# Performance work log

Measured on AMD Instinct MI355X. Metric: run time of the kernel, lower is better.

## Reference

```python
import jax, jax.numpy as jnp
import numpy as np

# static config (matches init_kwargs)
E = 1280          # n_embed
L = 4             # n_layer
NH = 16           # n_heads
D = E // NH       # head_dim = 80
M = 5120          # n_mlp
O = 2048          # n_output_embed
MS = 2            # spatial_merge_size
NGPS = 48         # sqrt(num_position_embeddings)
GRID_T, GRID_H, GRID_W = 1, 32, 32
N_IMG = 2
SPP = GRID_T * GRID_H * GRID_W   # 1024 tokens per image
S = N_IMG * SPP                  # 2048 total tokens
H4 = E * MS * MS                 # merger hidden = 5120
IN_PATCH = 3 * 2 * 16 * 16       # 1536
DS_IDX = [1, 2]


def _ln(x, w, b, eps=1e-6):
    m = x.mean(-1, keepdims=True)
    v = ((x - m) ** 2).mean(-1, keepdims=True)
    return (x - m) / jnp.sqrt(v + eps) * w + b


def _pos_embed_interp(pos_emb):
    # bilinear interpolation of the 48x48 learned grid to GRID_HxGRID_W, per image
    hi = jnp.linspace(0.0, NGPS - 1.0, GRID_H)
    wi = jnp.linspace(0.0, NGPS - 1.0, GRID_W)
    hf = hi.astype(jnp.int32); wf = wi.astype(jnp.int32)
    hc = jnp.minimum(hf + 1, NGPS - 1); wc = jnp.minimum(wf + 1, NGPS - 1)
    dh = hi - hf; dw = wi - wf
    idx = [(hf[:, None] * NGPS + wf[None]).ravel(), (hf[:, None] * NGPS + wc[None]).ravel(),
           (hc[:, None] * NGPS + wf[None]).ravel(), (hc[:, None] * NGPS + wc[None]).ravel()]
    wts = [((1 - dh)[:, None] * (1 - dw)[None]).ravel(), ((1 - dh)[:, None] * dw[None]).ravel(),
           (dh[:, None] * (1 - dw)[None]).ravel(), (dh[:, None] * dw[None]).ravel()]
    pe = sum(pos_emb[i] * w[:, None] for i, w in zip(idx, wts))  # [h*w, E]
    pe = jnp.tile(pe, (GRID_T, 1))
    # spatial-merge permutation: (t, h/m, m, w/m, m) -> (t, h/m, w/m, m, m)
    pe = pe.reshape(GRID_T, GRID_H // MS, MS, GRID_W // MS, MS, E).transpose(0, 1, 3, 2, 4, 5).reshape(-1, E)
    return jnp.tile(pe, (N_IMG, 1))  # [S, E]


def _rotary_freqs():
    dim = D // 2  # VisionRotaryEmbedding dim = 40
    inv = 1.0 / (10000.0 ** (jnp.arange(0, dim, 2, dtype=jnp.float32) / dim))  # [D//4]
    hp = jnp.broadcast_to(jnp.arange(GRID_H)[:, None], (GRID_H, GRID_W))
    hp = hp.reshape(GRID_H // MS, MS, GRID_W // MS, MS).transpose(0, 2, 1, 3).ravel()
    wp = jnp.broadcast_to(jnp.arange(GRID_W)[None, :], (GRID_H, GRID_W))
    wp = wp.reshape(GRID_H // MS, MS, GRID_W // MS, MS).transpose(0, 2, 1, 3).ravel()
    pos = jnp.stack([hp, wp], -1)            # [h*w, 2]
    pos = jnp.tile(pos, (GRID_T, 1))
    pos = jnp.tile(pos, (N_IMG, 1))          # [S, 2]
    table = jnp.arange(max(GRID_H, GRID_W), dtype=jnp.float32)[:, None] * inv[None]  # [G, D//4]
    return table[pos].reshape(S, -1)         # [S, D//2] (h-freqs || w-freqs)


def _rope(t, cos, sin):
    # t: [S, NH, D]; cos/sin: [S, 1, D]; applied in float32 as in the source
    t1, t2 = jnp.split(t, 2, axis=-1)
    rot = jnp.concatenate([-t2, t1], -1)
    return (t.astype(jnp.float32) * cos + rot.astype(jnp.float32) * sin).astype(t.dtype)


def _attn(x, qkv_w, qkv_b, pw, pb, cos, sin, mask):
    qkv = (x @ qkv_w.T + qkv_b).reshape(S, 3, NH, D)
    q, k, v = qkv[:, 0], qkv[:, 1], qkv[:, 2]
    q = _rope(q, cos, sin)
    k = _rope(k, cos, sin)
    scores = jnp.einsum('shd,thd->hst', q, k) / np.sqrt(D).astype(np.float32) + mask
    p = jax.nn.softmax(scores.astype(jnp.float32), axis=-1).astype(q.dtype)
    o = jnp.einsum('hst,thd->shd', p, v).reshape(S, E)
    return o @ pw.T + pb


def _merger(x, ln_w, ln_b, f1w, f1b, f2w, f2b, post):
    if post:
        x = _ln(x.reshape(-1, H4), ln_w, ln_b)
    else:
        x = _ln(x, ln_w, ln_b).reshape(-1, H4)
    h = jax.nn.gelu(x @ f1w.T + f1b, approximate=False)  # nn.GELU() exact
    return h @ f2w.T + f2b


def setup_inputs() -> dict:
    key = jax.random.key(0)
    ks = iter(jax.random.split(key, 24))
    n = lambda s: jax.random.normal(next(ks), s, dtype=jnp.float32) * 0.02
    return {
        'x': jax.random.normal(next(ks), (S, IN_PATCH), dtype=jnp.float32),
        'patch_w': n((E, IN_PATCH)), 'patch_b': jnp.zeros((E,), jnp.float32),
        'pos_emb': n((NGPS * NGPS, E)),
        'ln1_w': jnp.ones((L, E), jnp.float32), 'ln1_b': jnp.zeros((L, E), jnp.float32),
        'ln2_w': jnp.ones((L, E), jnp.float32), 'ln2_b': jnp.zeros((L, E), jnp.float32),
        'qkv_w': n((L, 3 * E, E)), 'qkv_b': jnp.zeros((L, 3 * E), jnp.float32),
        'attn_proj_w': n((L, E, E)), 'attn_proj_b': jnp.zeros((L, E), jnp.float32),
        'fc1_w': n((L, M, E)), 'fc1_b': jnp.zeros((L, M), jnp.float32),
        'fc2_w': n((L, E, M)), 'fc2_b': jnp.zeros((L, E), jnp.float32),
        'm_ln_w': jnp.ones((E,), jnp.float32), 'm_ln_b': jnp.zeros((E,), jnp.float32),
        'm_fc1_w': n((H4, H4)), 'm_fc1_b': jnp.zeros((H4,), jnp.float32),
        'm_fc2_w': n((O, H4)), 'm_fc2_b': jnp.zeros((O,), jnp.float32),
        'ds_ln_w': jnp.ones((2, H4), jnp.float32), 'ds_ln_b': jnp.zeros((2, H4), jnp.float32),
        'ds_fc1_w': n((2, H4, H4)), 'ds_fc1_b': jnp.zeros((2, H4), jnp.float32),
        'ds_fc2_w': n((2, O, H4)), 'ds_fc2_b': jnp.zeros((2, O), jnp.float32),
    }


def reference(x, patch_w, patch_b, pos_emb, ln1_w, ln1_b, ln2_w, ln2_b,
              qkv_w, qkv_b, attn_proj_w, attn_proj_b, fc1_w, fc1_b, fc2_w, fc2_b,
              m_ln_w, m_ln_b, m_fc1_w, m_fc1_b, m_fc2_w, m_fc2_b,
              ds_ln_w, ds_ln_b, ds_fc1_w, ds_fc1_b, ds_fc2_w, ds_fc2_b):
    # patch embed (Conv3d with kernel==stride == per-patch linear)
    h = x @ patch_w.T + patch_b                      # [S, E]
    h = h + _pos_embed_interp(pos_emb)
    freqs = _rotary_freqs()                          # [S, D//2]
    cos = jnp.concatenate([jnp.cos(freqs)] * 2, -1)[:, None, :]  # [S,1,D]
    sin = jnp.concatenate([jnp.sin(freqs)] * 2, -1)[:, None, :]
    img = jnp.arange(S) // SPP                       # cu_seqlens block-diagonal mask
    mask = jnp.where(img[:, None] == img[None, :], 0.0, jnp.finfo(jnp.float32).min)
    ds_feats = []
    for l in range(L):
        h = h + _attn(_ln(h, ln1_w[l], ln1_b[l]), qkv_w[l], qkv_b[l],
                      attn_proj_w[l], attn_proj_b[l], cos, sin, mask)
        hn = _ln(h, ln2_w[l], ln2_b[l])
        h = h + (jax.nn.gelu(hn @ fc1_w[l].T + fc1_b[l], approximate=True) @ fc2_w[l].T + fc2_b[l])
        if l in DS_IDX:
            j = DS_IDX.index(l)
            ds_feats.append(_merger(h, ds_ln_w[j], ds_ln_b[j], ds_fc1_w[j], ds_fc1_b[j],
                                    ds_fc2_w[j], ds_fc2_b[j], post=True))
    main = _merger(h, m_ln_w, m_ln_b, m_fc1_w, m_fc1_b, m_fc2_w, m_fc2_b, post=False)
    return jnp.stack([main] + ds_feats, 0)           # [3, S//4, O]
```

## Files before the change

### kernel.cpp

```cpp
#include <hip/hip_runtime.h>
#include <hip/hip_bf16.h>
#include <cstdio>
#include <cstdint>

#define E_    1280
#define L_    4
#define NH_   16
#define D_    80
#define DP_   96
#define MLP_  5120
#define O_    2048
#define S_    2048
#define H4_   5120
#define INP_  1536

typedef __attribute__((ext_vector_type(4))) float f32x4;
typedef __attribute__((ext_vector_type(8))) short short8v;
typedef __attribute__((ext_vector_type(4))) short short4v;

__device__ __forceinline__ short f2bf(float f){
  uint32_t u = __float_as_uint(f);
  uint32_t r = (u + 0x7FFFu + ((u >> 16) & 1u)) >> 16;
  return (short)r;
}
__device__ __forceinline__ float bf2f(short s){
  return __uint_as_float(((uint32_t)(uint16_t)s) << 16);
}
__device__ __forceinline__ float gelu_tanh(float x){
  return 0.5f*x*(1.f + tanhf(0.7978845608028654f*(x + 0.044715f*x*x*x)));
}
__device__ __forceinline__ float gelu_erf(float x){
  return 0.5f*x*(1.f + erff(x*0.7071067811865476f));
}
__device__ __forceinline__ void token_hw(int t, int& hc, int& wc){
  hc = ((t>>1)&1) + ((t>>6)<<1);
  wc = (t&1)      + (((t>>2)&15)<<1);
}

__device__ __forceinline__ void gload16(const short* g, short* l){
  __builtin_amdgcn_global_load_lds((const __attribute__((address_space(1))) void*)g,
                                   (__attribute__((address_space(3))) void*)l, 16, 0, 0);
}

struct CvtSeg { const float* src; short* dst; long long n; };
struct CvtP { CvtSeg s[10]; long long tot; };

__global__ __launch_bounds__(256)
void cvtall_k(CvtP p)
{
  const long long stride = (long long)gridDim.x*256*8;
  for (long long i = ((long long)blockIdx.x*256 + threadIdx.x)*8; i < p.tot; i += stride){
    long long off = i; int si = 0;
    #pragma unroll
    for (int k=0;k<9;k++){ if (off >= p.s[si].n){ off -= p.s[si].n; si++; } }
    const float* src = p.s[si].src + off;
    short* dst = p.s[si].dst + off;
    float4 v0 = *(const float4*)(src);
    float4 v1 = *(const float4*)(src+4);
    short8v w;
    w[0]=f2bf(v0.x); w[1]=f2bf(v0.y); w[2]=f2bf(v0.z); w[3]=f2bf(v0.w);
    w[4]=f2bf(v1.x); w[5]=f2bf(v1.y); w[6]=f2bf(v1.z); w[7]=f2bf(v1.w);
    *(short8v*)dst = w;
  }
}

struct Gemm2P {
  const short* A; const short* B; void* C;
  const float* bias;
  short* part;
  int lda, ldb, ldc, M, N, K;
  float scale;
  long long aOffH, aOffI, bOffH, bOffI, cOffH, cOffI;
  int nImg, kSplit;
};

template<int EPI, bool RES, bool CF32, bool SPLIT>
__global__ __launch_bounds__(256)
void gemm2_k(Gemm2P p)
{
  __shared__ short As[3][4096];
  __shared__ short Bs[3][4096];

  int z = blockIdx.z, ks = 0;
  if constexpr (SPLIT){ ks = z % p.kSplit; z /= p.kSplit; }
  const int hI = z / p.nImg, iI = z % p.nImg;
  const long long aB = (long long)hI*p.aOffH + (long long)iI*p.aOffI;
  const long long bB = (long long)hI*p.bOffH + (long long)iI*p.bOffI;
  const long long cB = (long long)hI*p.cOffH + (long long)iI*p.cOffI;

  const int nwg = gridDim.x*gridDim.y;
  const int orig = blockIdx.y*gridDim.x + blockIdx.x;
  const int q8 = nwg >> 3, r8 = nwg & 7;
  const int xcd = orig & 7, oidx = orig >> 3;
  const int wg = (xcd < r8 ? xcd*(q8+1) : r8*(q8+1) + (xcd-r8)*q8) + oidx;
  const int nt = wg % gridDim.x, mt = wg / gridDim.x;

  const int tid = threadIdx.x, lane = tid & 63, wv = tid >> 6;

  const int sr = lane >> 2;
  const int sc = (lane & 3) * 8;
  const int Kp  = SPLIT ? p.K / p.kSplit : p.K;
  const int kBeg = SPLIT ? ks * Kp : 0;
  int ra0 = mt*128 + (wv*2+0)*16 + sr; if (ra0 >= p.M) ra0 = p.M-1;
  int ra1 = mt*128 + (wv*2+1)*16 + sr; if (ra1 >= p.M) ra1 = p.M-1;
  int rb0 = nt*128 + (wv*2+0)*16 + sr; if (rb0 >= p.N) rb0 = p.N-1;
  int rb1 = nt*128 + (wv*2+1)*16 + sr; if (rb1 >= p.N) rb1 = p.N-1;
  const short* pa0 = p.A + aB + (long long)ra0*p.lda + sc + kBeg;
  const short* pa1 = p.A + aB + (long long)ra1*p.lda + sc + kBeg;
  const short* pb0 = p.B + bB + (long long)rb0*p.ldb + sc + kBeg;
  const short* pb1 = p.B + bB + (long long)rb1*p.ldb + sc + kBeg;
  const int so0 = (wv*2+0)*512;
  const int so1 = (wv*2+1)*512;

  const int fr = lane & 15, fo = (lane >> 4) * 8;
  const int wr = (wv >> 1) * 64, wc = (wv & 1) * 64;

  f32x4 acc[4][4] = {};

  auto stage = [&](int buf, int t){
    const int k0 = t << 5;
    gload16(pa0 + k0, &As[buf][so0]);
    gload16(pa1 + k0, &As[buf][so1]);
    gload16(pb0 + k0, &Bs[buf][so0]);
    gload16(pb1 + k0, &Bs[buf][so1]);
  };

  const int ntile = Kp >> 5;
  stage(0, 0);
  if (ntile > 1) stage(1, 1);
  for (int t = 0; t < ntile; t++){
    const int cur = t % 3;
    if (t + 1 < ntile) { asm volatile("s_waitcnt vmcnt(4)" ::: "memory"); }
    else               { asm volatile("s_waitcnt vmcnt(0)" ::: "memory"); }
    __builtin_amdgcn_s_barrier();
    asm volatile("" ::: "memory");
    short8v a[4], b[4];
    #pragma unroll
    for (int i=0;i<4;i++){
      a[i] = *(const short8v*)&As[cur][(wr + i*16 + fr)*32 + fo];
      b[i] = *(const short8v*)&Bs[cur][(wc + i*16 + fr)*32 + fo];
    }
    if (t + 2 < ntile) stage((t+2)%3, t+2);
    #pragma unroll
    for (int i=0;i<4;i++)
      #pragma unroll
      for (int j=0;j<4;j++)
        acc[i][j] = __builtin_amdgcn_mfma_f32_16x16x32_bf16(a[i], b[j], acc[i][j], 0, 0, 0);
  }

  #pragma unroll
  for (int i=0;i<4;i++){
    #pragma unroll
    for (int j=0;j<4;j++){
      #pragma unroll
      for (int r=0;r<4;r++){
        const int row = mt*128 + wr + i*16 + (lane>>4)*4 + r;
        const int col = nt*128 + wc + j*16 + fr;
        if (row < p.M && col < p.N){
          float v = acc[i][j][r];
          if constexpr (SPLIT){
            p.part[((long long)ks*p.M + row)*p.N + col] = f2bf(v);
          } else {
            if (p.bias) v += p.bias[col];
            if constexpr (EPI==1) v = gelu_tanh(v);
            if constexpr (EPI==2) v = gelu_erf(v);
            if constexpr (EPI==3) v *= p.scale;
            const long long off = cB + (long long)row*p.ldc + col;
            if constexpr (RES)  v += ((const float*)p.C)[off];
            if constexpr (CF32) ((float*)p.C)[off] = v;
            else                ((short*)p.C)[off] = f2bf(v);
          }
        }
      }
    }
  }
}

template<int EPI, bool RES, bool CF32>
__global__ __launch_bounds__(256)
void reduce_k(const short* __restrict__ part, int kSplit, long long MN, int N,
              const float* __restrict__ bias, void* __restrict__ C)
{
  const long long i = ((long long)blockIdx.x*256 + threadIdx.x)*8;
  if (i >= MN) return;
  float v[8];
  { short8v pv = *(const short8v*)(part + i);
    #pragma unroll
    for (int e=0;e<8;e++) v[e] = bf2f(pv[e]); }
  for (int ks = 1; ks < kSplit; ks++){
    short8v pv = *(const short8v*)(part + (long long)ks*MN + i);
    #pragma unroll
    for (int e=0;e<8;e++) v[e] += bf2f(pv[e]);
  }
  if (bias){
    const int col = (int)(i % N);
    #pragma unroll
    for (int e=0;e<8;e++) v[e] += bias[col+e];
  }
  #pragma unroll
  for (int e=0;e<8;e++){
    if constexpr (EPI==1) v[e] = gelu_tanh(v[e]);
    if constexpr (EPI==2) v[e] = gelu_erf(v[e]);
  }
  if constexpr (RES){
    const float* cp = (const float*)C + i;
    #pragma unroll
    for (int e=0;e<8;e++) v[e] += cp[e];
  }
  if constexpr (CF32){
    float4 o0 = {v[0],v[1],v[2],v[3]}, o1 = {v[4],v[5],v[6],v[7]};
    *(float4*)((float*)C + i) = o0;
    *(float4*)((float*)C + i + 4) = o1;
  } else {
    short8v o;
    #pragma unroll
    for (int e=0;e<8;e++) o[e] = f2bf(v[e]);
    *(short8v*)((short*)C + i) = o;
  }
}

__global__ __launch_bounds__(256)
void redln_k(const short* __restrict__ part, long long MN, const float* __restrict__ bias,
             float* __restrict__ h, const float* __restrict__ lnw, const float* __restrict__ lnb,
             short* __restrict__ aln)
{
  __shared__ float red[8];
  const int row = blockIdx.x, tid = threadIdx.x;
  float4 vals[2];
  float s = 0.f, sq = 0.f;
  #pragma unroll
  for (int it=0; it<2; it++){
    const int c = tid*4 + it*1024;
    if (c < E_){
      float4 v = *(const float4*)(h + (long long)row*E_ + c);
      const float4 b = *(const float4*)(bias + c);
      v.x += b.x; v.y += b.y; v.z += b.z; v.w += b.w;
      #pragma unroll
      for (int ks=0; ks<4; ks++){
        short4v pv = *(const short4v*)(part + (long long)ks*MN + (long long)row*E_ + c);
        v.x += bf2f(pv[0]); v.y += bf2f(pv[1]); v.z += bf2f(pv[2]); v.w += bf2f(pv[3]);
      }
      *(float4*)(h + (long long)row*E_ + c) = v;
      vals[it] = v;
      s  += v.x+v.y+v.z+v.w;
      sq += v.x*v.x+v.y*v.y+v.z*v.z+v.w*v.w;
    }
  }
  #pragma unroll
  for (int m=32;m;m>>=1){ s += __shfl_xor(s,m,64); sq += __shfl_xor(sq,m,64); }
  const int wv = tid>>6, lane = tid&63;
  if (lane==0){ red[wv]=s; red[4+wv]=sq; }
  __syncthreads();
  s  = red[0]+red[1]+red[2]+red[3];
  sq = red[4]+red[5]+red[6]+red[7];
  const float mean = s / (float)E_;
  const float var  = sq / (float)E_ - mean*mean;
  const float rs   = rsqrtf(var + 1e-6f);
  #pragma unroll
  for (int it=0; it<2; it++){
    const int c = tid*4 + it*1024;
    if (c < E_){
      const float4 v = vals[it];
      const float4 gw = *(const float4*)(lnw + c);
      const float4 bw = *(const float4*)(lnb + c);
      short4v o;
      o[0] = f2bf((v.x-mean)*rs*gw.x + bw.x);
      o[1] = f2bf((v.y-mean)*rs*gw.y + bw.y);
      o[2] = f2bf((v.z-mean)*rs*gw.z + bw.z);
      o[3] = f2bf((v.w-mean)*rs*gw.w + bw.w);
      *(short4v*)(aln + (long long)row*E_ + c) = o;
    }
  }
}

__global__ __launch_bounds__(256)
void fattn_k(const short* __restrict__ qh, const short* __restrict__ kh,
             const short* __restrict__ vt, short* __restrict__ o2)
{
  __shared__ short Ps[4][16*136];

  const int qt = blockIdx.x, h = blockIdx.y, img = blockIdx.z;
  const int tid = threadIdx.x, lane = tid & 63, wv = tid >> 6;
  const int fr = lane & 15, fo = (lane >> 4) * 8, g = lane >> 4;

  const short* qp = qh + ((long long)h*S_ + img*1024 + qt*64 + wv*16)*DP_;
  const short* kp = kh + ((long long)h*S_ + img*1024)*DP_;
  const short* vp = vt + ((long long)(h*2 + img))*80*1024;
  short* Pw = &Ps[wv][0];

  short8v q[3];
  #pragma unroll
  for (int t3=0;t3<3;t3++)
    q[t3] = *(const short8v*)(qp + (long long)fr*DP_ + t3*32 + fo);

  float m_[4], l_[4];
  f32x4 ao[5] = {};
  #pragma unroll
  for (int r=0;r<4;r++){ m_[r] = -3.0e38f; l_[r] = 0.f; }

  for (int t = 0; t < 8; t++){
    f32x4 sc[8] = {};
    #pragma unroll
    for (int j=0;j<8;j++){
      #pragma unroll
      for (int t3=0;t3<3;t3++){
        const short8v kb = *(const short8v*)(kp + (long long)(t*128 + j*16 + fr)*DP_ + t3*32 + fo);
        sc[j] = __builtin_amdgcn_mfma_f32_16x16x32_bf16(q[t3], kb, sc[j], 0,0,0);
      }
    }
    #pragma unroll
    for (int j=0;j<8;j++) sc[j] *= 0.11180339887498949f;

    #pragma unroll
    for (int r=0;r<4;r++){
      float mx = sc[0][r];
      #pragma unroll
      for (int j=1;j<8;j++) mx = fmaxf(mx, sc[j][r]);
      mx = fmaxf(mx, __shfl_xor(mx, 1, 64));
      mx = fmaxf(mx, __shfl_xor(mx, 2, 64));
      mx = fmaxf(mx, __shfl_xor(mx, 4, 64));
      mx = fmaxf(mx, __shfl_xor(mx, 8, 64));
      const float mn = fmaxf(m_[r], mx);
      const float al = __expf(m_[r] - mn);
      float ts = 0.f;
      #pragma unroll
      for (int j=0;j<8;j++){
        const float pv = __expf(sc[j][r] - mn);
        sc[j][r] = pv;
        ts += pv;
      }
      ts += __shfl_xor(ts, 1, 64);
      ts += __shfl_xor(ts, 2, 64);
      ts += __shfl_xor(ts, 4, 64);
      ts += __shfl_xor(ts, 8, 64);
      l_[r] = l_[r]*al + ts;
      m_[r] = mn;
      #pragma unroll
      for (int n=0;n<5;n++) ao[n][r] *= al;
      const int prow = g*4 + r;
      #pragma unroll
      for (int j=0;j<8;j++) Pw[prow*136 + j*16 + fr] = f2bf(sc[j][r]);
    }
    asm volatile("s_waitcnt lgkmcnt(0)" ::: "memory");
    __builtin_amdgcn_sched_barrier(0);

    #pragma unroll
    for (int t4=0;t4<4;t4++){
      const short8v pa = *(const short8v*)&Pw[fr*136 + t4*32 + fo];
      #pragma unroll
      for (int n=0;n<5;n++){
        const short8v vb = *(const short8v*)(vp + (long long)(n*16 + fr)*1024 + t*128 + t4*32 + fo);
        ao[n] = __builtin_amdgcn_mfma_f32_16x16x32_bf16(pa, vb, ao[n], 0,0,0);
      }
    }
  }

  short* op = o2 + ((long long)(img*1024 + qt*64 + wv*16))*E_ + h*80;
  #pragma unroll
  for (int r=0;r<4;r++){
    const float inv = 1.f / l_[r];
    const int row = g*4 + r;
    #pragma unroll
    for (int n=0;n<5;n++)
      op[(long long)row*E_ + n*16 + fr] = f2bf(ao[n][r] * inv);
  }
}

__global__ __launch_bounds__(256)
void ln_k(const float* __restrict__ X, const float* __restrict__ g, const float* __restrict__ bta,
          short* __restrict__ Y, int Cn)
{
  __shared__ float red[8];
  const int row = blockIdx.x;
  const float* x = X + (long long)row*Cn;
  short* y = Y + (long long)row*Cn;
  float s = 0.f, sq = 0.f;
  for (int c = threadIdx.x*4; c < Cn; c += 1024){
    float4 v = *(const float4*)(x + c);
    s  += v.x+v.y+v.z+v.w;
    sq += v.x*v.x+v.y*v.y+v.z*v.z+v.w*v.w;
  }
  #pragma unroll
  for (int m=32;m;m>>=1){ s += __shfl_xor(s,m,64); sq += __shfl_xor(sq,m,64); }
  const int wv = threadIdx.x>>6, lane = threadIdx.x&63;
  if (lane==0){ red[wv]=s; red[4+wv]=sq; }
  __syncthreads();
  s  = red[0]+red[1]+red[2]+red[3];
  sq = red[4]+red[5]+red[6]+red[7];
  const float mean = s / (float)Cn;
  const float var  = sq / (float)Cn - mean*mean;
  const float rs   = rsqrtf(var + 1e-6f);
  for (int c = threadIdx.x*4; c < Cn; c += 1024){
    float4 v  = *(const float4*)(x + c);
    float4 gw = *(const float4*)(g + c);
    float4 bw = *(const float4*)(bta + c);
    short4v o;
    o[0] = f2bf((v.x-mean)*rs*gw.x + bw.x);
    o[1] = f2bf((v.y-mean)*rs*gw.y + bw.y);
    o[2] = f2bf((v.z-mean)*rs*gw.z + bw.z);
    o[3] = f2bf((v.w-mean)*rs*gw.w + bw.w);
    *(short4v*)(y + c) = o;
  }
}

__global__ __launch_bounds__(256)
void rope_k(const short* __restrict__ qkv, short* __restrict__ qh,
            short* __restrict__ kh, short* __restrict__ vt)
{
  const int idx = blockIdx.x*256 + threadIdx.x;
  if (idx >= S_*NH_*40) return;
  const int d0 = idx % 40;
  const int h  = (idx / 40) % NH_;
  const int s  = idx / (40*NH_);
  const int t  = s & 1023, img = s >> 10;
  int hc, wc; token_hw(t, hc, wc);
  const int j  = d0 % 20;
  const float invf = exp2f(-0.66438561897747f * (float)j);
  const float pos  = (float)((d0 < 20) ? hc : wc);
  float sn, cs; sincosf(pos * invf, &sn, &cs);
  const short* base = qkv + (long long)s*3840 + h*80;
  const float q1 = bf2f(base[d0]),      q2 = bf2f(base[d0+40]);
  const float k1 = bf2f(base[1280+d0]), k2 = bf2f(base[1280+d0+40]);
  const long long qo = ((long long)h*S_ + s)*DP_;
  qh[qo + d0]    = f2bf(q1*cs - q2*sn);
  qh[qo + d0+40] = f2bf(q2*cs + q1*sn);
  kh[qo + d0]    = f2bf(k1*cs - k2*sn);
  kh[qo + d0+40] = f2bf(k2*cs + k1*sn);
  if (d0 < 16){ qh[qo + 80 + d0] = 0; kh[qo + 80 + d0] = 0; }
  const long long vo = (((long long)h*2 + img)*80)*1024 + t;
  vt[vo + (long long)d0*1024]      = base[2560+d0];
  vt[vo + (long long)(d0+40)*1024] = base[2560+d0+40];
}

__global__ __launch_bounds__(256)
void posadd_k(float* __restrict__ h, const float* __restrict__ pe)
{
  const int idx = blockIdx.x*256 + threadIdx.x;
  if (idx >= S_*(E_/4)) return;
  const int c4 = idx % (E_/4), s = idx / (E_/4);
  const int e = c4*4;
  const int t = s & 1023;
  int hc, wc; token_hw(t, hc, wc);
  const float hi = (float)hc * (47.f/31.f);
  const float wi = (float)wc * (47.f/31.f);
  int hf = (int)hi; float dh = hi - (float)hf; int h2 = min(hf+1, 47);
  int wf = (int)wi; float dw = wi - (float)wf; int w2 = min(wf+1, 47);
  const float w00=(1.f-dh)*(1.f-dw), w01=(1.f-dh)*dw, w10=dh*(1.f-dw), w11=dh*dw;
  const float4 a = *(const float4*)(pe + ((long long)(hf*48+wf))*E_ + e);
  const float4 b = *(const float4*)(pe + ((long long)(hf*48+w2))*E_ + e);
  const float4 c = *(const float4*)(pe + ((long long)(h2*48+wf))*E_ + e);
  const float4 d = *(const float4*)(pe + ((long long)(h2*48+w2))*E_ + e);
  float* out = h + (long long)s*E_ + e;
  float4 o = *(float4*)out;
  o.x += w00*a.x + w01*b.x + w10*c.x + w11*d.x;
  o.y += w00*a.y + w01*b.y + w10*c.y + w11*d.y;
  o.z += w00*a.z + w01*b.z + w10*c.z + w11*d.z;
  o.w += w00*a.w + w01*b.w + w10*c.w + w11*d.w;
  *(float4*)out = o;
}

static Gemm2P mk(const short* A, const short* B, void* C, const float* bias,
                 int lda, int ldb, int ldc, int M, int N, int K, float scale = 1.f)
{
  Gemm2P p{}; p.A=A; p.B=B; p.C=C; p.bias=bias; p.part=nullptr;
  p.lda=lda; p.ldb=ldb; p.ldc=ldc; p.M=M; p.N=N; p.K=K; p.scale=scale;
  p.aOffH=p.aOffI=p.bOffH=p.bOffI=p.cOffH=p.cOffI=0; p.nImg=1; p.kSplit=1;
  return p;
}

extern "C" void kernel_launch(void* const* d_in, const int* in_sizes, int n_in,
                              void* d_out, int out_size, void* d_ws, size_t ws_size,
                              hipStream_t stream)
{
  const float* x           = (const float*)d_in[0];
  const float* patch_w     = (const float*)d_in[1];
  const float* patch_b     = (const float*)d_in[2];
  const float* pos_emb     = (const float*)d_in[3];
  const float* ln1_w       = (const float*)d_in[4];
  const float* ln1_b       = (const float*)d_in[5];
  const float* ln2_w       = (const float*)d_in[6];
  const float* ln2_b       = (const float*)d_in[7];
  const float* qkv_w       = (const float*)d_in[8];
  const float* qkv_b       = (const float*)d_in[9];
  const float* attn_proj_w = (const float*)d_in[10];
  const float* attn_proj_b = (const float*)d_in[11];
  const float* fc1_w       = (const float*)d_in[12];
  const float* fc1_b       = (const float*)d_in[13];
  const float* fc2_w       = (const float*)d_in[14];
  const float* fc2_b       = (const float*)d_in[15];
  const float* m_ln_w      = (const float*)d_in[16];
  const float* m_ln_b      = (const float*)d_in[17];
  const float* m_fc1_w     = (const float*)d_in[18];
  const float* m_fc1_b     = (const float*)d_in[19];
  const float* m_fc2_w     = (const float*)d_in[20];
  const float* m_fc2_b     = (const float*)d_in[21];
  const float* ds_ln_w     = (const float*)d_in[22];
  const float* ds_ln_b     = (const float*)d_in[23];
  const float* ds_fc1_w    = (const float*)d_in[24];
  const float* ds_fc1_b    = (const float*)d_in[25];
  const float* ds_fc2_w    = (const float*)d_in[26];
  const float* ds_fc2_b    = (const float*)d_in[27];
  float* out = (float*)d_out;

  char* wsp = (char*)d_ws;
  auto alloc = [&](size_t bytes)->char*{
    char* p = wsp; wsp += (bytes + 255) & ~(size_t)255; return p;
  };
  float* h    = (float*)alloc((size_t)S_*E_*4);
  short* qkvb = (short*)alloc((size_t)S_*3840*2);
  short* aln  = (short*)alloc((size_t)S_*E_*2);
  short* qh   = (short*)alloc((size_t)NH_*S_*DP_*2);
  short* kh   = (short*)alloc((size_t)NH_*S_*DP_*2 + 4096);
  short* vt   = (short*)alloc((size_t)NH_*2*D_*1024*2 + 4096);
  short* part = (short*)alloc((size_t)24*1024*1024);
  short* o2   = (short*)alloc((size_t)S_*E_*2);
  short* ffn  = (short*)alloc((size_t)S_*MLP_*2);
  short* xb    = (short*)alloc((size_t)S_*INP_*2);
  short* pwB   = (short*)alloc((size_t)E_*INP_*2);
  short* qkvwB = (short*)alloc((size_t)L_*3840*E_*2);
  short* prwB  = (short*)alloc((size_t)L_*E_*E_*2);
  short* f1wB  = (short*)alloc((size_t)L_*MLP_*E_*2);
  short* f2wB  = (short*)alloc((size_t)L_*E_*MLP_*2);
  short* mf1B  = (short*)alloc((size_t)H4_*H4_*2);
  short* mf2B  = (short*)alloc((size_t)O_*H4_*2);
  short* df1B  = (short*)alloc((size_t)2*H4_*H4_*2);
  short* df2B  = (short*)alloc((size_t)2*O_*H4_*2);
  size_t need = (size_t)(wsp - (char*)d_ws);
  if (need > ws_size){
    fprintf(stderr, "kernel_launch: ws too small: need %zu have %zu\n", need, ws_size);
    return;
  }
  short* dsln = qkvb;

  const dim3 B256(256);

  { CvtP cp{};
    cp.s[0] = { x,         xb,    (long long)S_*INP_ };
    cp.s[1] = { patch_w,   pwB,   (long long)E_*INP_ };
    cp.s[2] = { qkv_w,     qkvwB, (long long)L_*3840*E_ };
    cp.s[3] = { attn_proj_w, prwB, (long long)L_*E_*E_ };
    cp.s[4] = { fc1_w,     f1wB,  (long long)L_*MLP_*E_ };
    cp.s[5] = { fc2_w,     f2wB,  (long long)L_*E_*MLP_ };
    cp.s[6] = { m_fc1_w,   mf1B,  (long long)H4_*H4_ };
    cp.s[7] = { m_fc2_w,   mf2B,  (long long)O_*H4_ };
    cp.s[8] = { ds_fc1_w,  df1B,  (long long)2*H4_*H4_ };
    cp.s[9] = { ds_fc2_w,  df2B,  (long long)2*O_*H4_ };
    cp.tot = 0;
    for (int i=0;i<10;i++) cp.tot += cp.s[i].n;
    cvtall_k<<<2048, B256, 0, stream>>>(cp); }

  auto G = [](int M, int N, int ks = 1){
    return dim3((unsigned)((N+127)/128), (unsigned)((M+127)/128), (unsigned)ks);
  };
  auto RG = [](long long MN){ return dim3((unsigned)((MN/8 + 255)/256)); };

  { Gemm2P pp = mk(xb, pwB, h, nullptr, INP_, INP_, E_, S_, E_, INP_);
    pp.part = part; pp.kSplit = 4;
    gemm2_k<0,false,true,true><<<G(S_,E_,4),B256,0,stream>>>(pp);
    reduce_k<0,false,true><<<RG((long long)S_*E_),B256,0,stream>>>(part, 4, (long long)S_*E_, E_, patch_b, h); }
  posadd_k<<<(S_*(E_/4)+255)/256, B256, 0, stream>>>(h, pos_emb);
  ln_k<<<S_, B256, 0, stream>>>(h, ln1_w, ln1_b, aln, E_);

  for (int l = 0; l < L_; l++){
    { Gemm2P pp = mk(aln, qkvwB + (size_t)l*3840*E_, qkvb, qkv_b + l*3840, E_, E_, 3840, S_, 3840, E_);
      gemm2_k<0,false,false,false><<<G(S_,3840),B256,0,stream>>>(pp); }
    rope_k<<<(S_*NH_*40+255)/256, B256, 0, stream>>>(qkvb, qh, kh, vt);
    fattn_k<<<dim3(16,16,2), B256, 0, stream>>>(qh, kh, vt, o2);
    { Gemm2P pp = mk(o2, prwB + (size_t)l*E_*E_, nullptr, nullptr, E_, E_, E_, S_, E_, E_);
      pp.part = part; pp.kSplit = 4;
      gemm2_k<0,false,true,true><<<G(S_,E_,4),B256,0,stream>>>(pp);
      redln_k<<<S_, B256, 0, stream>>>(part, (long long)S_*E_, attn_proj_b + l*E_,
                                       h, ln2_w + l*E_, ln2_b + l*E_, aln); }

    { Gemm2P pp = mk(aln, f1wB + (size_t)l*MLP_*E_, ffn, fc1_b + l*MLP_, E_, E_, MLP_, S_, MLP_, E_);
      gemm2_k<1,false,false,false><<<G(S_,MLP_),B256,0,stream>>>(pp); }
    { Gemm2P pp = mk(ffn, f2wB + (size_t)l*E_*MLP_, nullptr, nullptr, MLP_, MLP_, E_, S_, E_, MLP_);
      pp.part = part; pp.kSplit = 4;
      gemm2_k<0,false,true,true><<<G(S_,E_,4),B256,0,stream>>>(pp);
      const float* nw = (l < 3) ? (ln1_w + (l+1)*E_) : m_ln_w;
      const float* nb = (l < 3) ? (ln1_b + (l+1)*E_) : m_ln_b;
      redln_k<<<S_, B256, 0, stream>>>(part, (long long)S_*E_, fc2_b + l*E_, h, nw, nb, aln); }

    if (l == 1 || l == 2){
      const int j = l - 1;
      ln_k<<<512, B256, 0, stream>>>(h, ds_ln_w + (size_t)j*H4_, ds_ln_b + (size_t)j*H4_, dsln, H4_);
      { Gemm2P pp = mk(dsln, df1B + (size_t)j*H4_*H4_, ffn, nullptr, H4_, H4_, H4_, 512, H4_, H4_);
        pp.part = part; pp.kSplit = 4;
        gemm2_k<0,false,false,true><<<G(512,H4_,4),B256,0,stream>>>(pp);
        reduce_k<2,false,false><<<RG((long long)512*H4_),B256,0,stream>>>(part, 4, (long long)512*H4_, H4_, ds_fc1_b + (size_t)j*H4_, ffn); }
      { Gemm2P pp = mk(ffn, df2B + (size_t)j*O_*H4_, out + (size_t)(1+j)*512*O_, nullptr, H4_, H4_, O_, 512, O_, H4_);
        pp.part = part; pp.kSplit = 8;
        gemm2_k<0,false,true,true><<<G(512,O_,8),B256,0,stream>>>(pp);
        reduce_k<0,false,true><<<RG((long long)512*O_),B256,0,stream>>>(part, 8, (long long)512*O_, O_, ds_fc2_b + (size_t)j*O_, out + (size_t)(1+j)*512*O_); }
    }
  }

  { Gemm2P pp = mk(aln, mf1B, ffn, nullptr, H4_, H4_, H4_, 512, H4_, H4_);
    pp.part = part; pp.kSplit = 4;
    gemm2_k<0,false,false,true><<<G(512,H4_,4),B256,0,stream>>>(pp);
    reduce_k<2,false,false><<<RG((long long)512*H4_),B256,0,stream>>>(part, 4, (long long)512*H4_, H4_, m_fc1_b, ffn); }
  { Gemm2P pp = mk(ffn, mf2B, out, nullptr, H4_, H4_, O_, 512, O_, H4_);
    pp.part = part; pp.kSplit = 8;
    gemm2_k<0,false,true,true><<<G(512,O_,8),B256,0,stream>>>(pp);
    reduce_k<0,false,true><<<RG((long long)512*O_),B256,0,stream>>>(part, 8, (long long)512*O_, O_, m_fc2_b, out); }
}
```

Baseline: 1.779 ms.

## Split-K the QKV and FC1 GEMMs and split weight conversion per tensor

QKV and FC1 projections now run as 2-way split-K GEMMs writing bf16 partials, followed by a reduce kernel that applies bias (and GELU for FC1). The partial buffer is doubled to hold them. The single fused fp32->bf16 conversion kernel is replaced by one launch per tensor, and RoPE uses the fast __sincosf intrinsic. The aim is more parallelism and simpler conversion indexing, at the cost of extra partial-sum memory traffic, extra launches, and reduced sincos accuracy.

```diff
diff --git a/kernel.cpp b/kernel.cpp
--- a/kernel.cpp
+++ b/kernel.cpp
@@ -42,25 +42,17 @@
                                    (__attribute__((address_space(3))) void*)l, 16, 0, 0);
 }
 
-struct CvtSeg { const float* src; short* dst; long long n; };
-struct CvtP { CvtSeg s[10]; long long tot; };
-
-__global__ __launch_bounds__(256)
-void cvtall_k(CvtP p)
+__global__ __launch_bounds__(256)
+void cvt_k(const float* __restrict__ src, short* __restrict__ dst, long long n)
 {
   const long long stride = (long long)gridDim.x*256*8;
-  for (long long i = ((long long)blockIdx.x*256 + threadIdx.x)*8; i < p.tot; i += stride){
-    long long off = i; int si = 0;
-    #pragma unroll
-    for (int k=0;k<9;k++){ if (off >= p.s[si].n){ off -= p.s[si].n; si++; } }
-    const float* src = p.s[si].src + off;
-    short* dst = p.s[si].dst + off;
-    float4 v0 = *(const float4*)(src);
-    float4 v1 = *(const float4*)(src+4);
+  for (long long i = ((long long)blockIdx.x*256 + threadIdx.x)*8; i < n; i += stride){
+    float4 v0 = *(const float4*)(src+i);
+    float4 v1 = *(const float4*)(src+i+4);
     short8v w;
     w[0]=f2bf(v0.x); w[1]=f2bf(v0.y); w[2]=f2bf(v0.z); w[3]=f2bf(v0.w);
     w[4]=f2bf(v1.x); w[5]=f2bf(v1.y); w[6]=f2bf(v1.z); w[7]=f2bf(v1.w);
-    *(short8v*)dst = w;
+    *(short8v*)(dst+i) = w;
   }
 }
 
@@ -417,7 +409,8 @@
   const int j  = d0 % 20;
   const float invf = exp2f(-0.66438561897747f * (float)j);
   const float pos  = (float)((d0 < 20) ? hc : wc);
-  float sn, cs; sincosf(pos * invf, &sn, &cs);
+  float sn, cs;
+  __sincosf(pos * invf, &sn, &cs);
   const short* base = qkv + (long long)s*3840 + h*80;
   const float q1 = bf2f(base[d0]),      q2 = bf2f(base[d0+40]);
   const float k1 = bf2f(base[1280+d0]), k2 = bf2f(base[1280+d0+40]);
@@ -512,7 +505,7 @@
   short* qh   = (short*)alloc((size_t)NH_*S_*DP_*2);
   short* kh   = (short*)alloc((size_t)NH_*S_*DP_*2 + 4096);
   short* vt   = (short*)alloc((size_t)NH_*2*D_*1024*2 + 4096);
-  short* part = (short*)alloc((size_t)24*1024*1024);
+  short* part = (short*)alloc((size_t)48*1024*1024);
   short* o2   = (short*)alloc((size_t)S_*E_*2);
   short* ffn  = (short*)alloc((size_t)S_*MLP_*2);
   short* xb    = (short*)alloc((size_t)S_*INP_*2);
@@ -533,21 +526,20 @@
   short* dsln = qkvb;
 
   const dim3 B256(256);
-
-  { CvtP cp{};
-    cp.s[0] = { x,         xb,    (long long)S_*INP_ };
-    cp.s[1] = { patch_w,   pwB,   (long long)E_*INP_ };
-    cp.s[2] = { qkv_w,     qkvwB, (long long)L_*3840*E_ };
-    cp.s[3] = { attn_proj_w, prwB, (long long)L_*E_*E_ };
-    cp.s[4] = { fc1_w,     f1wB,  (long long)L_*MLP_*E_ };
-    cp.s[5] = { fc2_w,     f2wB,  (long long)L_*E_*MLP_ };
-    cp.s[6] = { m_fc1_w,   mf1B,  (long long)H4_*H4_ };
-    cp.s[7] = { m_fc2_w,   mf2B,  (long long)O_*H4_ };
-    cp.s[8] = { ds_fc1_w,  df1B,  (long long)2*H4_*H4_ };
-    cp.s[9] = { ds_fc2_w,  df2B,  (long long)2*O_*H4_ };
-    cp.tot = 0;
-    for (int i=0;i<10;i++) cp.tot += cp.s[i].n;
-    cvtall_k<<<2048, B256, 0, stream>>>(cp); }
+  auto cvt = [&](const float* src, short* dst, long long n){
+    unsigned blk = (unsigned)min((long long)8192, (n/8 + 255)/256);
+    cvt_k<<<blk, B256, 0, stream>>>(src, dst, n);
+  };
+  cvt(x, xb, (long long)S_*INP_);
+  cvt(patch_w, pwB, (long long)E_*INP_);
+  cvt(qkv_w, qkvwB, (long long)L_*3840*E_);
+  cvt(attn_proj_w, prwB, (long long)L_*E_*E_);
+  cvt(fc1_w, f1wB, (long long)L_*MLP_*E_);
+  cvt(fc2_w, f2wB, (long long)L_*E_*MLP_);
+  cvt(m_fc1_w, mf1B, (long long)H4_*H4_);
+  cvt(m_fc2_w, mf2B, (long long)O_*H4_);
+  cvt(ds_fc1_w, df1B, (long long)2*H4_*H4_);
+  cvt(ds_fc2_w, df2B, (long long)2*O_*H4_);
 
   auto G = [](int M, int N, int ks = 1){
     return dim3((unsigned)((N+127)/128), (unsigned)((M+127)/128), (unsigned)ks);
@@ -562,8 +554,10 @@
   ln_k<<<S_, B256, 0, stream>>>(h, ln1_w, ln1_b, aln, E_);
 
   for (int l = 0; l < L_; l++){
-    { Gemm2P pp = mk(aln, qkvwB + (size_t)l*3840*E_, qkvb, qkv_b + l*3840, E_, E_, 3840, S_, 3840, E_);
-      gemm2_k<0,false,false,false><<<G(S_,3840),B256,0,stream>>>(pp); }
+    { Gemm2P pp = mk(aln, qkvwB + (size_t)l*3840*E_, qkvb, nullptr, E_, E_, 3840, S_, 3840, E_);
+      pp.part = part; pp.kSplit = 2;
+      gemm2_k<0,false,false,true><<<G(S_,3840,2),B256,0,stream>>>(pp);
+      reduce_k<0,false,false><<<RG((long long)S_*3840),B256,0,stream>>>(part, 2, (long long)S_*3840, 3840, qkv_b + l*3840, qkvb); }
     rope_k<<<(S_*NH_*40+255)/256, B256, 0, stream>>>(qkvb, qh, kh, vt);
     fattn_k<<<dim3(16,16,2), B256, 0, stream>>>(qh, kh, vt, o2);
     { Gemm2P pp = mk(o2, prwB + (size_t)l*E_*E_, nullptr, nullptr, E_, E_, E_, S_, E_, E_);
@@ -572,8 +566,10 @@
       redln_k<<<S_, B256, 0, stream>>>(part, (long long)S_*E_, attn_proj_b + l*E_,
                                        h, ln2_w + l*E_, ln2_b + l*E_, aln); }
 
-    { Gemm2P pp = mk(aln, f1wB + (size_t)l*MLP_*E_, ffn, fc1_b + l*MLP_, E_, E_, MLP_, S_, MLP_, E_);
-      gemm2_k<1,false,false,false><<<G(S_,MLP_),B256,0,stream>>>(pp); }
+    { Gemm2P pp = mk(aln, f1wB + (size_t)l*MLP_*E_, ffn, nullptr, E_, E_, MLP_, S_, MLP_, E_);
+      pp.part = part; pp.kSplit = 2;
+      gemm2_k<0,false,false,true><<<G(S_,MLP_,2),B256,0,stream>>>(pp);
+      reduce_k<1,false,false><<<RG((long long)S_*MLP_),B256,0,stream>>>(part, 2, (long long)S_*MLP_, MLP_, fc1_b + l*MLP_, ffn); }
     { Gemm2P pp = mk(ffn, f2wB + (size_t)l*E_*MLP_, nullptr, nullptr, MLP_, MLP_, E_, S_, E_, MLP_);
       pp.part = part; pp.kSplit = 4;
       gemm2_k<0,false,true,true><<<G(S_,E_,4),B256,0,stream>>>(pp);
```

Result: no change. 1.773 ms (-0.4%).
